# Kernel optimization log

Measured on AMD Instinct MI355X. Metric: run time of the kernel, lower is better.

The kernel has to match this reference:

```python
import jax, jax.numpy as jnp
import numpy as np

N_NODES = 50000
N_EDGES = 800000
IN_FEATS = 256
OUT_FEATS = 32
NUM_HEADS = 8
NUM_ETYPES = 5


def setup_inputs() -> dict:
    key = jax.random.key(0)
    k1, k2, k3, k4, k5, k6 = jax.random.split(key, 6)
    feat = jax.random.normal(k1, (N_NODES, IN_FEATS), dtype=jnp.float32)
    # xavier_normal-ish scale for fc weight [H*D, in]
    fc_w = jax.random.normal(k2, (NUM_HEADS * OUT_FEATS, IN_FEATS), dtype=jnp.float32) * 0.088
    edge_emb = jax.random.normal(k3, (NUM_ETYPES, NUM_HEADS), dtype=jnp.float32)
    e_feat = jax.random.randint(k4, (N_EDGES,), 0, NUM_ETYPES)
    src = jax.random.randint(k5, (N_EDGES,), 0, N_NODES)
    dst = jax.random.randint(k6, (N_EDGES,), 0, N_NODES)
    return {"feat": feat, "fc_w": fc_w, "edge_emb": edge_emb,
            "e_feat": e_feat, "src": src, "dst": dst}


def reference(feat, fc_w, edge_emb, e_feat, src, dst):
    N = feat.shape[0]
    H, D = NUM_HEADS, OUT_FEATS
    # fc: [N, in] @ [in, H*D] -> [N, H, D]
    feat_src = (feat @ fc_w.T).reshape(N, H, D)
    # per-edge, per-head logits from edge-type embedding: [E, H]
    e = edge_emb[e_feat]
    # edge_softmax: softmax over incoming edges of each dst node, per head
    m = jax.ops.segment_max(e, dst, num_segments=N)          # [N, H]
    ex = jnp.exp(e - m[dst])                                  # [E, H]
    denom = jax.ops.segment_sum(ex, dst, num_segments=N)     # [N, H]
    attn = ex / denom[dst]                                    # [E, H]
    # attn_sum: sum of attention weights arriving at each dst (== 1 w/o dropout)
    attn_sum = jax.ops.segment_sum(attn, dst, num_segments=N)  # [N, H]
    # weighted aggregation: sum_e attn_e * feat_src[src_e]
    msg = feat_src[src] * attn[:, :, None]                    # [E, H, D]
    agg = jax.ops.segment_sum(msg, dst, num_segments=N)      # [N, H, D]
    rst = agg / (attn_sum[:, :, None] + 1e-12)
    return rst, attn
```

## Files before the change

kernel.cpp:

```cpp
#include <hip/hip_runtime.h>

typedef unsigned short u16;
typedef unsigned int u32;
typedef __attribute__((ext_vector_type(8))) short bf16x8;
typedef __attribute__((ext_vector_type(4))) float f32x4;

#define NND 50000
#define NE 800000
#define NH 8
#define ND 32
#define NTY 5

__device__ inline u16 f2bf(float x){
  u32 u = __float_as_uint(x);
  return (u16)((u + 0x7FFFu + ((u >> 16) & 1u)) >> 16);
}

__global__ __launch_bounds__(512, 4) void gemm_k(const float* __restrict__ A,
                                                 const float* __restrict__ W,
                                                 u16* __restrict__ C, int M){
  __shared__ float As[128 * 64];
  __shared__ u16  Ws[256 * 64];
  const int tid  = threadIdx.x;
  const int m0   = blockIdx.x * 128;
  const int lane = tid & 63, wid = tid >> 6;
  const int wm = (wid >> 2) * 64, wn = (wid & 3) * 64;
  const int ml = lane & 15, quad = lane >> 4;

  f32x4 acc[4][4] = {};

  const int ra = tid >> 2, ca = (tid & 3) * 4;
  int rag = m0 + ra; if (rag >= M) rag = M - 1;
  const float* aRow = A + (size_t)rag * 256;
  const int rw = tid >> 1, hw = tid & 1;
  const float* wRow = W + (size_t)rw * 256;

  for (int k0 = 0; k0 < 256; k0 += 64){
    #pragma unroll
    for (int q = 0; q < 4; q++){
      float4 v = *(const float4*)(aRow + k0 + (ca + q) * 4);
      *(float4*)(As + ra * 64 + (((ca + q) ^ (ra & 15)) * 4)) = v;
    }
    #pragma unroll
    for (int q = 0; q < 4; q++){
      int ck = hw * 4 + q;
      float4 u0 = *(const float4*)(wRow + k0 + ck * 8);
      float4 u1 = *(const float4*)(wRow + k0 + ck * 8 + 4);
      ushort4 h0 = make_ushort4(f2bf(u0.x), f2bf(u0.y), f2bf(u0.z), f2bf(u0.w));
      ushort4 h1 = make_ushort4(f2bf(u1.x), f2bf(u1.y), f2bf(u1.z), f2bf(u1.w));
      int cp = ck ^ (rw & 7);
      *(ushort4*)(Ws + rw * 64 + cp * 8) = h0;
      *(ushort4*)(Ws + rw * 64 + cp * 8 + 4) = h1;
    }
    __syncthreads();
    #pragma unroll
    for (int kk = 0; kk < 64; kk += 32){
      bf16x8 af[4], wf[4];
      #pragma unroll
      for (int t = 0; t < 4; t++){
        int r = wm + t * 16 + ml;
        int c0 = (kk >> 2) + quad * 2;
        float4 x0 = *(const float4*)(As + r * 64 + (((c0    ) ^ (r & 15)) * 4));
        float4 x1 = *(const float4*)(As + r * 64 + (((c0 + 1) ^ (r & 15)) * 4));
        af[t] = (bf16x8){ (short)f2bf(x0.x), (short)f2bf(x0.y), (short)f2bf(x0.z), (short)f2bf(x0.w),
                          (short)f2bf(x1.x), (short)f2bf(x1.y), (short)f2bf(x1.z), (short)f2bf(x1.w) };
      }
      #pragma unroll
      for (int t = 0; t < 4; t++){
        int n = wn + t * 16 + ml;
        int c = (kk >> 3) + quad;
        wf[t] = *(const bf16x8*)(Ws + n * 64 + ((c ^ (n & 7)) * 8));
      }
      #pragma unroll
      for (int i = 0; i < 4; i++)
        #pragma unroll
        for (int j = 0; j < 4; j++)
          acc[i][j] = __builtin_amdgcn_mfma_f32_16x16x32_bf16(af[i], wf[j], acc[i][j], 0, 0, 0);
    }
    __syncthreads();
  }
  #pragma unroll
  for (int i = 0; i < 4; i++){
    #pragma unroll
    for (int rr = 0; rr < 4; rr++){
      int row = m0 + wm + i * 16 + quad * 4 + rr;
      if (row < M){
        u16* crow = C + (size_t)row * 256 + wn;
        #pragma unroll
        for (int j = 0; j < 4; j++)
          crow[j * 16 + ml] = f2bf(acc[i][j][rr]);
      }
    }
  }
}

__global__ __launch_bounds__(256) void count_k(const int* __restrict__ dst,
                                               int* __restrict__ deg,
                                               int* __restrict__ epos){
  int e = blockIdx.x * 256 + threadIdx.x;
  if (e < NE) epos[e] = atomicAdd(&deg[dst[e]], 1);
}

__global__ __launch_bounds__(256) void scan1_k(const int* __restrict__ deg,
                                               int* __restrict__ offs,
                                               int* __restrict__ bsum){
  __shared__ int lds[256];
  int b = blockIdx.x, tid = threadIdx.x;
  int base = b * 1024 + tid * 4;
  int d[4]; int tsum = 0;
  #pragma unroll
  for (int j = 0; j < 4; j++){
    int node = base + j;
    int v = (node < NND) ? deg[node] : 0;
    d[j] = tsum; tsum += v;
  }
  lds[tid] = tsum; __syncthreads();
  for (int off = 1; off < 256; off <<= 1){
    int v = (tid >= off) ? lds[tid - off] : 0;
    __syncthreads();
    lds[tid] += v;
    __syncthreads();
  }
  int excl = lds[tid] - tsum;
  #pragma unroll
  for (int j = 0; j < 4; j++)
    if (base + j < NND) offs[base + j] = excl + d[j];
  if (tid == 255) bsum[b] = lds[tid];
}

__global__ __launch_bounds__(64) void scan2_k(const int* __restrict__ bsum,
                                              int* __restrict__ bbase, int nb){
  __shared__ int l[64];
  int tid = threadIdx.x;
  int v = (tid < nb) ? bsum[tid] : 0;
  l[tid] = v; __syncthreads();
  for (int off = 1; off < 64; off <<= 1){
    int u = (tid >= off) ? l[tid - off] : 0;
    __syncthreads();
    l[tid] += u;
    __syncthreads();
  }
  bbase[tid] = l[tid] - v;
}

__global__ __launch_bounds__(256) void scatter_k(const int* __restrict__ dst,
                                                 const int* __restrict__ src,
                                                 const int* __restrict__ ef,
                                                 const int* __restrict__ epos,
                                                 const int* __restrict__ offs,
                                                 const int* __restrict__ bbase,
                                                 int* __restrict__ csr){
  int e = blockIdx.x * 256 + threadIdx.x;
  if (e >= NE) return;
  int d = dst[e];
  int pos = offs[d] + bbase[d >> 10] + epos[e];
  csr[pos] = src[e] | (ef[e] << 16);
}

__global__ __launch_bounds__(256) void nden_k(const int* __restrict__ csr,
                                              const int* __restrict__ offs,
                                              const int* __restrict__ bbase,
                                              const int* __restrict__ deg,
                                              const float* __restrict__ emb,
                                              float* __restrict__ rd){
  __shared__ float wl[40];
  int tid = threadIdx.x;
  if (tid < 40){
    int t = tid >> 3, h = tid & 7;
    float m = emb[h];
    for (int tt = 1; tt < NTY; ++tt) m = fmaxf(m, emb[tt * 8 + h]);
    wl[tid] = expf(emb[t * 8 + h] - m);
  }
  __syncthreads();
  int n = blockIdx.x * 256 + tid;
  if (n >= NND) return;
  int s = offs[n] + bbase[n >> 10];
  int dcnt = deg[n];
  float sum[8] = {0,0,0,0,0,0,0,0};
  for (int i = 0; i < dcnt; i++){
    int t = ((u32)csr[s + i]) >> 16;
    #pragma unroll
    for (int h = 0; h < 8; h++) sum[h] += wl[t * 8 + h];
  }
  #pragma unroll
  for (int h = 0; h < 8; h++)
    rd[(size_t)n * 8 + h] = (sum[h] > 0.f) ? (1.f / sum[h]) : 0.f;
}

__global__ __launch_bounds__(256) void attn_k(const int* __restrict__ dst,
                                              const int* __restrict__ ef,
                                              const float* __restrict__ rd,
                                              const float* __restrict__ emb,
                                              float* __restrict__ attn){
  __shared__ float wl[40];
  int tid = threadIdx.x;
  if (tid < 40){
    int t = tid >> 3, h = tid & 7;
    float m = emb[h];
    for (int tt = 1; tt < NTY; ++tt) m = fmaxf(m, emb[tt * 8 + h]);
    wl[tid] = expf(emb[t * 8 + h] - m);
  }
  __syncthreads();
  int e = blockIdx.x * 256 + tid;
  if (e >= NE) return;
  int d = dst[e], t = ef[e];
  float4 r0 = *(const float4*)(rd + (size_t)d * 8);
  float4 r1 = *(const float4*)(rd + (size_t)d * 8 + 4);
  const float* wr = wl + t * 8;
  *(float4*)(attn + (size_t)e * 8)     = make_float4(wr[0]*r0.x, wr[1]*r0.y, wr[2]*r0.z, wr[3]*r0.w);
  *(float4*)(attn + (size_t)e * 8 + 4) = make_float4(wr[4]*r1.x, wr[5]*r1.y, wr[6]*r1.z, wr[7]*r1.w);
}

__device__ inline void acc8(uint4 v, float wt, float* a){
  a[0] += wt * __uint_as_float(v.x << 16);
  a[1] += wt * __uint_as_float(v.x & 0xFFFF0000u);
  a[2] += wt * __uint_as_float(v.y << 16);
  a[3] += wt * __uint_as_float(v.y & 0xFFFF0000u);
  a[4] += wt * __uint_as_float(v.z << 16);
  a[5] += wt * __uint_as_float(v.z & 0xFFFF0000u);
  a[6] += wt * __uint_as_float(v.w << 16);
  a[7] += wt * __uint_as_float(v.w & 0xFFFF0000u);
}

__global__ __launch_bounds__(256) void agg_k(const u16* __restrict__ fsrc,
                                             const int* __restrict__ csr,
                                             const int* __restrict__ offs,
                                             const int* __restrict__ bbase,
                                             const int* __restrict__ deg,
                                             const float* __restrict__ emb,
                                             float* __restrict__ rst){
  __shared__ float wl[40];
  int tid = threadIdx.x;
  if (tid < 40){
    int t = tid >> 3, h = tid & 7;
    float m = emb[h];
    for (int tt = 1; tt < NTY; ++tt) m = fmaxf(m, emb[tt * 8 + h]);
    wl[tid] = expf(emb[t * 8 + h] - m);
  }
  __syncthreads();
  int node = blockIdx.x * 8 + (tid >> 5);
  int sl = tid & 31;
  int c = sl * 8;
  int h = sl >> 2;
  int s = offs[node] + bbase[node >> 10];
  int e = s + deg[node];
  float a[8] = {0,0,0,0,0,0,0,0};
  float ss = 0.f;
  int i = s;
  for (; i + 3 < e; i += 4){
    int p0 = csr[i], p1 = csr[i+1], p2 = csr[i+2], p3 = csr[i+3];
    uint4 v0 = *(const uint4*)(fsrc + (size_t)(p0 & 0xFFFF) * 256 + c);
    uint4 v1 = *(const uint4*)(fsrc + (size_t)(p1 & 0xFFFF) * 256 + c);
    uint4 v2 = *(const uint4*)(fsrc + (size_t)(p2 & 0xFFFF) * 256 + c);
    uint4 v3 = *(const uint4*)(fsrc + (size_t)(p3 & 0xFFFF) * 256 + c);
    float w0 = wl[(((u32)p0) >> 16) * 8 + h];
    float w1 = wl[(((u32)p1) >> 16) * 8 + h];
    float w2 = wl[(((u32)p2) >> 16) * 8 + h];
    float w3 = wl[(((u32)p3) >> 16) * 8 + h];
    acc8(v0, w0, a); acc8(v1, w1, a); acc8(v2, w2, a); acc8(v3, w3, a);
    ss += (w0 + w1) + (w2 + w3);
  }
  for (; i < e; i++){
    int p0 = csr[i];
    uint4 v0 = *(const uint4*)(fsrc + (size_t)(p0 & 0xFFFF) * 256 + c);
    float w0 = wl[(((u32)p0) >> 16) * 8 + h];
    acc8(v0, w0, a);
    ss += w0;
  }
  float inv = 1.0f / (ss + 1e-12f);
  float* orow = rst + (size_t)node * 256 + c;
  *(float4*)(orow)     = make_float4(a[0]*inv, a[1]*inv, a[2]*inv, a[3]*inv);
  *(float4*)(orow + 4) = make_float4(a[4]*inv, a[5]*inv, a[6]*inv, a[7]*inv);
}

extern "C" void kernel_launch(void* const* d_in, const int* in_sizes, int n_in,
                              void* d_out, int out_size, void* d_ws, size_t ws_size,
                              hipStream_t stream) {
  const float* feat = (const float*)d_in[0];
  const float* fcw  = (const float*)d_in[1];
  const float* emb  = (const float*)d_in[2];
  const int*   ef   = (const int*)d_in[3];
  const int*   src  = (const int*)d_in[4];
  const int*   dst  = (const int*)d_in[5];

  float* rst  = (float*)d_out;
  float* attn = (float*)d_out + (size_t)NND * NH * ND;

  char* ws = (char*)d_ws;
  size_t o = 0;
  u16* fsrc    = (u16*)(ws + o);   o += (size_t)NND * 256 * 2;
  int* csr     = (int*)(ws + o);   o += (size_t)NE * 4;
  int* epos    = (int*)(ws + o);   o += (size_t)NE * 4;
  int* offs    = (int*)(ws + o);   o += 200064;
  int* deg     = (int*)(ws + o);   o += 200064;
  float* rd    = (float*)(ws + o); o += (size_t)NND * NH * 4;
  int* bsum    = (int*)(ws + o);   o += 256;
  int* bbase   = (int*)(ws + o);   o += 256;

  hipMemsetAsync(deg, 0, (size_t)NND * 4, stream);

  gemm_k<<<391, 512, 0, stream>>>(feat, fcw, fsrc, NND);
  count_k<<<(NE + 255) / 256, 256, 0, stream>>>(dst, deg, epos);
  scan1_k<<<(NND + 1023) / 1024, 256, 0, stream>>>(deg, offs, bsum);
  scan2_k<<<1, 64, 0, stream>>>(bsum, bbase, (NND + 1023) / 1024);
  scatter_k<<<(NE + 255) / 256, 256, 0, stream>>>(dst, src, ef, epos, offs, bbase, csr);
  nden_k<<<(NND + 255) / 256, 256, 0, stream>>>(csr, offs, bbase, deg, emb, rd);
  attn_k<<<(NE + 255) / 256, 256, 0, stream>>>(dst, ef, rd, emb, attn);
  agg_k<<<NND / 8, 256, 0, stream>>>(fsrc, csr, offs, bbase, deg, emb, rst);
}
```

Measured before the change: 285.2 us.

## Restructure GEMM with pre-converted bf16 weights and fuse denominators into aggregation

A separate small kernel now converts the fc weights to bf16 once. The GEMM is restructured into 32-row tiles that stage the whole bf16 A row in LDS and read weights directly from global/L2, so it no longer converts W per block or loops over K with barriers. The per-node softmax denominator kernel is removed: the aggregation kernel, which already sums the weights, writes the reciprocal for the attention kernel, which now runs after it. Nontemporal loads/stores and __expf are added, trading exactness of exp and relying on L2 hits for weight fragments.

```diff
diff --git a/kernel.cpp b/kernel.cpp
--- a/kernel.cpp
+++ b/kernel.cpp
@@ -3,7 +3,9 @@
 typedef unsigned short u16;
 typedef unsigned int u32;
 typedef __attribute__((ext_vector_type(8))) short bf16x8;
+typedef __attribute__((ext_vector_type(8))) unsigned short u16x8;
 typedef __attribute__((ext_vector_type(4))) float f32x4;
+typedef __attribute__((ext_vector_type(4))) u32 u32x4;
 
 #define NND 50000
 #define NE 800000
@@ -16,74 +18,66 @@
   return (u16)((u + 0x7FFFu + ((u >> 16) & 1u)) >> 16);
 }
 
-__global__ __launch_bounds__(512, 4) void gemm_k(const float* __restrict__ A,
-                                                 const float* __restrict__ W,
+__global__ __launch_bounds__(256) void wcvt_k(const float* __restrict__ W,
+                                              u16* __restrict__ Wb){
+  int i = blockIdx.x * 256 + threadIdx.x;
+  f32x4 v = ((const f32x4*)W)[i];
+  ((ushort4*)Wb)[i] = make_ushort4(f2bf(v.x), f2bf(v.y), f2bf(v.z), f2bf(v.w));
+}
+
+__global__ __launch_bounds__(256, 4) void gemm_k(const float* __restrict__ A,
+                                                 const u16* __restrict__ Wb,
                                                  u16* __restrict__ C, int M){
-  __shared__ float As[128 * 64];
-  __shared__ u16  Ws[256 * 64];
+  __shared__ u16 As[32 * 256];
   const int tid  = threadIdx.x;
-  const int m0   = blockIdx.x * 128;
-  const int lane = tid & 63, wid = tid >> 6;
-  const int wm = (wid >> 2) * 64, wn = (wid & 3) * 64;
-  const int ml = lane & 15, quad = lane >> 4;
-
-  f32x4 acc[4][4] = {};
-
-  const int ra = tid >> 2, ca = (tid & 3) * 4;
-  int rag = m0 + ra; if (rag >= M) rag = M - 1;
-  const float* aRow = A + (size_t)rag * 256;
-  const int rw = tid >> 1, hw = tid & 1;
-  const float* wRow = W + (size_t)rw * 256;
-
-  for (int k0 = 0; k0 < 256; k0 += 64){
+  const int m0   = blockIdx.x * 32;
+  const int lane = tid & 63, w = tid >> 6;
+  const int wn   = w * 64;
+  const int ml   = lane & 15, quad = lane >> 4;
+
+  {
+    int row = tid >> 3;
+    int c0  = (tid & 7) * 4;
+    int rag = m0 + row; if (rag >= M) rag = M - 1;
+    const float* ar = A + (size_t)rag * 256;
     #pragma unroll
     for (int q = 0; q < 4; q++){
-      float4 v = *(const float4*)(aRow + k0 + (ca + q) * 4);
-      *(float4*)(As + ra * 64 + (((ca + q) ^ (ra & 15)) * 4)) = v;
+      int c = c0 + q;
+      f32x4 x0 = __builtin_nontemporal_load((const f32x4*)(ar + c * 8));
+      f32x4 x1 = __builtin_nontemporal_load((const f32x4*)(ar + c * 8 + 4));
+      u16x8 h = { f2bf(x0.x), f2bf(x0.y), f2bf(x0.z), f2bf(x0.w),
+                  f2bf(x1.x), f2bf(x1.y), f2bf(x1.z), f2bf(x1.w) };
+      *(u16x8*)(As + row * 256 + ((c ^ (row & 7)) * 8)) = h;
     }
-    #pragma unroll
-    for (int q = 0; q < 4; q++){
-      int ck = hw * 4 + q;
-      float4 u0 = *(const float4*)(wRow + k0 + ck * 8);
-      float4 u1 = *(const float4*)(wRow + k0 + ck * 8 + 4);
-      ushort4 h0 = make_ushort4(f2bf(u0.x), f2bf(u0.y), f2bf(u0.z), f2bf(u0.w));
-      ushort4 h1 = make_ushort4(f2bf(u1.x), f2bf(u1.y), f2bf(u1.z), f2bf(u1.w));
-      int cp = ck ^ (rw & 7);
-      *(ushort4*)(Ws + rw * 64 + cp * 8) = h0;
-      *(ushort4*)(Ws + rw * 64 + cp * 8 + 4) = h1;
+  }
+  __syncthreads();
+
+  f32x4 acc[2][4] = {};
+  const u16* wbase = Wb + (size_t)wn * 256;
+  #pragma unroll
+  for (int ks = 0; ks < 8; ks++){
+    bf16x8 af[2], wf[4];
+    #pragma unroll
+    for (int t = 0; t < 2; t++){
+      int r = t * 16 + ml;
+      int c = ks * 4 + quad;
+      af[t] = *(const bf16x8*)(As + r * 256 + ((c ^ (r & 7)) * 8));
     }
-    __syncthreads();
-    #pragma unroll
-    for (int kk = 0; kk < 64; kk += 32){
-      bf16x8 af[4], wf[4];
+    #pragma unroll
+    for (int t = 0; t < 4; t++)
+      wf[t] = *(const bf16x8*)(wbase + (size_t)(t * 16 + ml) * 256 + ks * 32 + quad * 8);
+    #pragma unroll
+    for (int i = 0; i < 2; i++)
       #pragma unroll
-      for (int t = 0; t < 4; t++){
-        int r = wm + t * 16 + ml;
-        int c0 = (kk >> 2) + quad * 2;
-        float4 x0 = *(const float4*)(As + r * 64 + (((c0    ) ^ (r & 15)) * 4));
-        float4 x1 = *(const float4*)(As + r * 64 + (((c0 + 1) ^ (r & 15)) * 4));
-        af[t] = (bf16x8){ (short)f2bf(x0.x), (short)f2bf(x0.y), (short)f2bf(x0.z), (short)f2bf(x0.w),
-                          (short)f2bf(x1.x), (short)f2bf(x1.y), (short)f2bf(x1.z), (short)f2bf(x1.w) };
-      }
-      #pragma unroll
-      for (int t = 0; t < 4; t++){
-        int n = wn + t * 16 + ml;
-        int c = (kk >> 3) + quad;
-        wf[t] = *(const bf16x8*)(Ws + n * 64 + ((c ^ (n & 7)) * 8));
-      }
-      #pragma unroll
-      for (int i = 0; i < 4; i++)
-        #pragma unroll
-        for (int j = 0; j < 4; j++)
-          acc[i][j] = __builtin_amdgcn_mfma_f32_16x16x32_bf16(af[i], wf[j], acc[i][j], 0, 0, 0);
-    }
-    __syncthreads();
-  }
-  #pragma unroll
-  for (int i = 0; i < 4; i++){
+      for (int j = 0; j < 4; j++)
+        acc[i][j] = __builtin_amdgcn_mfma_f32_16x16x32_bf16(af[i], wf[j], acc[i][j], 0, 0, 0);
+  }
+
+  #pragma unroll
+  for (int i = 0; i < 2; i++){
     #pragma unroll
     for (int rr = 0; rr < 4; rr++){
-      int row = m0 + wm + i * 16 + quad * 4 + rr;
+      int row = m0 + i * 16 + quad * 4 + rr;
       if (row < M){
         u16* crow = C + (size_t)row * 256 + wn;
         #pragma unroll
@@ -98,7 +92,10 @@
                                                int* __restrict__ deg,
                                                int* __restrict__ epos){
   int e = blockIdx.x * 256 + threadIdx.x;
-  if (e < NE) epos[e] = atomicAdd(&deg[dst[e]], 1);
+  if (e < NE){
+    int p = atomicAdd(&deg[dst[e]], 1);
+    __builtin_nontemporal_store(p, epos + e);
+  }
 }
 
 __global__ __launch_bounds__(256) void scan1_k(const int* __restrict__ deg,
@@ -157,34 +154,74 @@
   csr[pos] = src[e] | (ef[e] << 16);
 }
 
-__global__ __launch_bounds__(256) void nden_k(const int* __restrict__ csr,
-                                              const int* __restrict__ offs,
-                                              const int* __restrict__ bbase,
-                                              const int* __restrict__ deg,
-                                              const float* __restrict__ emb,
-                                              float* __restrict__ rd){
+__device__ inline void acc8(u32x4 v, float wt, float* a){
+  a[0] += wt * __uint_as_float(v.x << 16);
+  a[1] += wt * __uint_as_float(v.x & 0xFFFF0000u);
+  a[2] += wt * __uint_as_float(v.y << 16);
+  a[3] += wt * __uint_as_float(v.y & 0xFFFF0000u);
+  a[4] += wt * __uint_as_float(v.z << 16);
+  a[5] += wt * __uint_as_float(v.z & 0xFFFF0000u);
+  a[6] += wt * __uint_as_float(v.w << 16);
+  a[7] += wt * __uint_as_float(v.w & 0xFFFF0000u);
+}
+
+__global__ __launch_bounds__(256) void agg_k(const u16* __restrict__ fsrc,
+                                             const int* __restrict__ csr,
+                                             const int* __restrict__ offs,
+                                             const int* __restrict__ bbase,
+                                             const int* __restrict__ deg,
+                                             const float* __restrict__ emb,
+                                             float* __restrict__ rst,
+                                             float* __restrict__ rd){
   __shared__ float wl[40];
   int tid = threadIdx.x;
   if (tid < 40){
     int t = tid >> 3, h = tid & 7;
     float m = emb[h];
     for (int tt = 1; tt < NTY; ++tt) m = fmaxf(m, emb[tt * 8 + h]);
-    wl[tid] = expf(emb[t * 8 + h] - m);
+    wl[tid] = __expf(emb[t * 8 + h] - m);
   }
   __syncthreads();
-  int n = blockIdx.x * 256 + tid;
-  if (n >= NND) return;
-  int s = offs[n] + bbase[n >> 10];
-  int dcnt = deg[n];
-  float sum[8] = {0,0,0,0,0,0,0,0};
-  for (int i = 0; i < dcnt; i++){
-    int t = ((u32)csr[s + i]) >> 16;
-    #pragma unroll
-    for (int h = 0; h < 8; h++) sum[h] += wl[t * 8 + h];
-  }
-  #pragma unroll
-  for (int h = 0; h < 8; h++)
-    rd[(size_t)n * 8 + h] = (sum[h] > 0.f) ? (1.f / sum[h]) : 0.f;
+  int node = blockIdx.x * 8 + (tid >> 5);
+  int sl = tid & 31;
+  int c = sl * 8;
+  int h = sl >> 2;
+  int s = offs[node] + bbase[node >> 10];
+  int e = s + deg[node];
+  float a[8] = {0,0,0,0,0,0,0,0};
+  float ss = 0.f;
+  int i = s;
+  for (; i + 3 < e; i += 4){
+    int p0 = __builtin_nontemporal_load(csr + i);
+    int p1 = __builtin_nontemporal_load(csr + i + 1);
+    int p2 = __builtin_nontemporal_load(csr + i + 2);
+    int p3 = __builtin_nontemporal_load(csr + i + 3);
+    u32x4 v0 = *(const u32x4*)(fsrc + (size_t)(p0 & 0xFFFF) * 256 + c);
+    u32x4 v1 = *(const u32x4*)(fsrc + (size_t)(p1 & 0xFFFF) * 256 + c);
+    u32x4 v2 = *(const u32x4*)(fsrc + (size_t)(p2 & 0xFFFF) * 256 + c);
+    u32x4 v3 = *(const u32x4*)(fsrc + (size_t)(p3 & 0xFFFF) * 256 + c);
+    float w0 = wl[(((u32)p0) >> 16) * 8 + h];
+    float w1 = wl[(((u32)p1) >> 16) * 8 + h];
+    float w2 = wl[(((u32)p2) >> 16) * 8 + h];
+    float w3 = wl[(((u32)p3) >> 16) * 8 + h];
+    acc8(v0, w0, a); acc8(v1, w1, a); acc8(v2, w2, a); acc8(v3, w3, a);
+    ss += (w0 + w1) + (w2 + w3);
+  }
+  for (; i < e; i++){
+    int p0 = __builtin_nontemporal_load(csr + i);
+    u32x4 v0 = *(const u32x4*)(fsrc + (size_t)(p0 & 0xFFFF) * 256 + c);
+    float w0 = wl[(((u32)p0) >> 16) * 8 + h];
+    acc8(v0, w0, a);
+    ss += w0;
+  }
+  float inv = 1.0f / (ss + 1e-12f);
+  float* orow = rst + (size_t)node * 256 + c;
+  f32x4 o0 = { a[0]*inv, a[1]*inv, a[2]*inv, a[3]*inv };
+  f32x4 o1 = { a[4]*inv, a[5]*inv, a[6]*inv, a[7]*inv };
+  __builtin_nontemporal_store(o0, (f32x4*)orow);
+  __builtin_nontemporal_store(o1, (f32x4*)(orow + 4));
+  if ((sl & 3) == 0)
+    rd[(size_t)node * 8 + h] = (ss > 0.f) ? (1.0f / ss) : 0.f;
 }
 
 __global__ __launch_bounds__(256) void attn_k(const int* __restrict__ dst,
@@ -198,79 +235,19 @@
     int t = tid >> 3, h = tid & 7;
     float m = emb[h];
     for (int tt = 1; tt < NTY; ++tt) m = fmaxf(m, emb[tt * 8 + h]);
-    wl[tid] = expf(emb[t * 8 + h] - m);
+    wl[tid] = __expf(emb[t * 8 + h] - m);
   }
   __syncthreads();
   int e = blockIdx.x * 256 + tid;
   if (e >= NE) return;
   int d = dst[e], t = ef[e];
-  float4 r0 = *(const float4*)(rd + (size_t)d * 8);
-  float4 r1 = *(const float4*)(rd + (size_t)d * 8 + 4);
+  f32x4 r0 = *(const f32x4*)(rd + (size_t)d * 8);
+  f32x4 r1 = *(const f32x4*)(rd + (size_t)d * 8 + 4);
   const float* wr = wl + t * 8;
-  *(float4*)(attn + (size_t)e * 8)     = make_float4(wr[0]*r0.x, wr[1]*r0.y, wr[2]*r0.z, wr[3]*r0.w);
-  *(float4*)(attn + (size_t)e * 8 + 4) = make_float4(wr[4]*r1.x, wr[5]*r1.y, wr[6]*r1.z, wr[7]*r1.w);
-}
-
-__device__ inline void acc8(uint4 v, float wt, float* a){
-  a[0] += wt * __uint_as_float(v.x << 16);
-  a[1] += wt * __uint_as_float(v.x & 0xFFFF0000u);
-  a[2] += wt * __uint_as_float(v.y << 16);
-  a[3] += wt * __uint_as_float(v.y & 0xFFFF0000u);
-  a[4] += wt * __uint_as_float(v.z << 16);
-  a[5] += wt * __uint_as_float(v.z & 0xFFFF0000u);
-  a[6] += wt * __uint_as_float(v.w << 16);
-  a[7] += wt * __uint_as_float(v.w & 0xFFFF0000u);
-}
-
-__global__ __launch_bounds__(256) void agg_k(const u16* __restrict__ fsrc,
-                                             const int* __restrict__ csr,
-                                             const int* __restrict__ offs,
-                                             const int* __restrict__ bbase,
-                                             const int* __restrict__ deg,
-                                             const float* __restrict__ emb,
-                                             float* __restrict__ rst){
-  __shared__ float wl[40];
-  int tid = threadIdx.x;
-  if (tid < 40){
-    int t = tid >> 3, h = tid & 7;
-    float m = emb[h];
-    for (int tt = 1; tt < NTY; ++tt) m = fmaxf(m, emb[tt * 8 + h]);
-    wl[tid] = expf(emb[t * 8 + h] - m);
-  }
-  __syncthreads();
-  int node = blockIdx.x * 8 + (tid >> 5);
-  int sl = tid & 31;
-  int c = sl * 8;
-  int h = sl >> 2;
-  int s = offs[node] + bbase[node >> 10];
-  int e = s + deg[node];
-  float a[8] = {0,0,0,0,0,0,0,0};
-  float ss = 0.f;
-  int i = s;
-  for (; i + 3 < e; i += 4){
-    int p0 = csr[i], p1 = csr[i+1], p2 = csr[i+2], p3 = csr[i+3];
-    uint4 v0 = *(const uint4*)(fsrc + (size_t)(p0 & 0xFFFF) * 256 + c);
-    uint4 v1 = *(const uint4*)(fsrc + (size_t)(p1 & 0xFFFF) * 256 + c);
-    uint4 v2 = *(const uint4*)(fsrc + (size_t)(p2 & 0xFFFF) * 256 + c);
-    uint4 v3 = *(const uint4*)(fsrc + (size_t)(p3 & 0xFFFF) * 256 + c);
-    float w0 = wl[(((u32)p0) >> 16) * 8 + h];
-    float w1 = wl[(((u32)p1) >> 16) * 8 + h];
-    float w2 = wl[(((u32)p2) >> 16) * 8 + h];
-    float w3 = wl[(((u32)p3) >> 16) * 8 + h];
-    acc8(v0, w0, a); acc8(v1, w1, a); acc8(v2, w2, a); acc8(v3, w3, a);
-    ss += (w0 + w1) + (w2 + w3);
-  }
-  for (; i < e; i++){
-    int p0 = csr[i];
-    uint4 v0 = *(const uint4*)(fsrc + (size_t)(p0 & 0xFFFF) * 256 + c);
-    float w0 = wl[(((u32)p0) >> 16) * 8 + h];
-    acc8(v0, w0, a);
-    ss += w0;
-  }
-  float inv = 1.0f / (ss + 1e-12f);
-  float* orow = rst + (size_t)node * 256 + c;
-  *(float4*)(orow)     = make_float4(a[0]*inv, a[1]*inv, a[2]*inv, a[3]*inv);
-  *(float4*)(orow + 4) = make_float4(a[4]*inv, a[5]*inv, a[6]*inv, a[7]*inv);
+  f32x4 o0 = { wr[0]*r0.x, wr[1]*r0.y, wr[2]*r0.z, wr[3]*r0.w };
+  f32x4 o1 = { wr[4]*r1.x, wr[5]*r1.y, wr[6]*r1.z, wr[7]*r1.w };
+  __builtin_nontemporal_store(o0, (f32x4*)(attn + (size_t)e * 8));
+  __builtin_nontemporal_store(o1, (f32x4*)(attn + (size_t)e * 8 + 4));
 }
 
 extern "C" void kernel_launch(void* const* d_in, const int* in_sizes, int n_in,
@@ -294,17 +271,18 @@
   int* offs    = (int*)(ws + o);   o += 200064;
   int* deg     = (int*)(ws + o);   o += 200064;
   float* rd    = (float*)(ws + o); o += (size_t)NND * NH * 4;
+  u16* Wb      = (u16*)(ws + o);   o += (size_t)256 * 256 * 2;
   int* bsum    = (int*)(ws + o);   o += 256;
   int* bbase   = (int*)(ws + o);   o += 256;
 
-  hipMemsetAsync(deg, 0, (size_t)NND * 4, stream);
-
-  gemm_k<<<391, 512, 0, stream>>>(feat, fcw, fsrc, NND);
+  (void)hipMemsetAsync(deg, 0, (size_t)NND * 4, stream);
+
+  wcvt_k<<<64, 256, 0, stream>>>(fcw, Wb);
+  gemm_k<<<(NND + 31) / 32, 256, 0, stream>>>(feat, Wb, fsrc, NND);
   count_k<<<(NE + 255) / 256, 256, 0, stream>>>(dst, deg, epos);
   scan1_k<<<(NND + 1023) / 1024, 256, 0, stream>>>(deg, offs, bsum);
   scan2_k<<<1, 64, 0, stream>>>(bsum, bbase, (NND + 1023) / 1024);
   scatter_k<<<(NE + 255) / 256, 256, 0, stream>>>(dst, src, ef, epos, offs, bbase, csr);
-  nden_k<<<(NND + 255) / 256, 256, 0, stream>>>(csr, offs, bbase, deg, emb, rd);
+  agg_k<<<NND / 8, 256, 0, stream>>>(fsrc, csr, offs, bbase, deg, emb, rst, rd);
   attn_k<<<(NE + 255) / 256, 256, 0, stream>>>(dst, ef, rd, emb, attn);
-  agg_k<<<NND / 8, 256, 0, stream>>>(fsrc, csr, offs, bbase, deg, emb, rst);
-}
+}
```

After: 295.1 us. 1.03x slower.
